# Performance work log

Measured on AMD Instinct MI355X. Metric: run time of the kernel, lower is better.

Reference implementation:

```python
import jax, jax.numpy as jnp
import numpy as np

B, S, J, D = 64, 2048, 25, 3
FEAT_DIM = 128
COMPUTED = 12  # pos(3) + vel(3) + acc(3) + angles(3)
IN_MLP = COMPUTED * J  # 300
HID = FEAT_DIM * 2     # 256
CONN = np.array([(0, 1), (1, 5), (1, 6), (5, 7), (7, 9), (6, 8), (8, 10),
                 (1, 11), (1, 12), (11, 13), (13, 15), (12, 14), (14, 16)], dtype=np.int32)


def setup_inputs() -> dict:
    key = jax.random.key(0)
    ks = jax.random.split(key, 8)
    return {
        "poses": jax.random.normal(ks[0], (B, S, J, D), dtype=jnp.float32),
        "W1": jax.random.normal(ks[1], (IN_MLP, HID), dtype=jnp.float32) * 0.05,
        "b1": jnp.zeros((HID,), jnp.float32),
        "gamma": jnp.ones((HID,), jnp.float32),
        "beta": jnp.zeros((HID,), jnp.float32),
        "running_mean": jnp.zeros((HID,), jnp.float32),
        "running_var": jnp.ones((HID,), jnp.float32),
        "W2": jax.random.normal(ks[2], (HID, FEAT_DIM), dtype=jnp.float32) * 0.05,
        "b2": jnp.zeros((FEAT_DIM,), jnp.float32),
        "joint_weights": jnp.ones((J,), jnp.float32),
    }


def reference(poses, W1, b1, gamma, beta, running_mean, running_var, W2, b2, joint_weights):
    b, s, j, d = poses.shape
    # --- root-centering + max-distance normalization ---
    p = poses - poses[:, :, 0:1, :]
    dist = jnp.linalg.norm(p, axis=-1, keepdims=True)           # [B,S,J,1]
    max_dist = jnp.max(dist, axis=2, keepdims=True)             # [B,S,1,1]
    p = p / (max_dist + 1e-8)
    # --- velocity / acceleration (zero-padded first frames) ---
    zpad = jnp.zeros_like(p[:, :1])
    vel = jnp.concatenate([zpad, p[:, 1:] - p[:, :-1]], axis=1)
    acc = jnp.concatenate([zpad, vel[:, 1:] - vel[:, :-1]], axis=1)
    # --- joint angles: vectorized gather + normalize + acos (replaces B*S*13 python loop) ---
    v1 = p[:, :, CONN[:, 1], :] - p[:, :, CONN[:, 0], :]        # [B,S,13,3]
    vnorm = jnp.maximum(jnp.linalg.norm(v1, axis=-1, keepdims=True), 1e-12)  # F.normalize eps
    ang = jnp.arccos(jnp.clip(v1 / vnorm, -1.0, 1.0))           # [B,S,13,3]
    ang = ang.reshape(b, s, -1)                                 # [B,S,39]
    pad = jnp.zeros((b, s, j * 3 - ang.shape[-1]), ang.dtype)   # pad to J*3=75
    angles = jnp.concatenate([ang, pad], axis=-1).reshape(b, s, j, 3)
    # --- combine, weight, project ---
    feat = jnp.concatenate([p, vel, acc, angles], axis=-1)      # [B,S,J,12]
    feat = feat * joint_weights.reshape(1, 1, j, 1)
    x = feat.reshape(b * s, -1)                                 # [B*S,300]
    x = x @ W1 + b1
    x = gamma * (x - running_mean) / jnp.sqrt(running_var + 1e-5) + beta  # BN eval mode
    x = jax.nn.relu(x)                                          # dropout = identity (eval)
    x = x @ W2 + b2
    return x.reshape(b, s, -1)                                  # [B,S,128]
```

## Files before the change

kernel.cpp:

```cpp
#include <hip/hip_runtime.h>
#include <stdint.h>


#define S_    2048
#define MT_   64
#define TPB   512
#define HID_  256
#define OUT_  128

typedef __attribute__((ext_vector_type(8))) _Float16 half8;
typedef __attribute__((ext_vector_type(4))) float    floatx4;
typedef __attribute__((ext_vector_type(4))) float    f4_t;

#define C0M 0x0ECDB118675110ULL
#define C1M 0x0FDECBA9786540ULL

__device__ __forceinline__ float facos(float x) {
    float ax = fabsf(x);
    float p = fmaf(ax, -0.0187293f, 0.0742610f);
    p = fmaf(ax, p, -0.2121144f);
    p = fmaf(ax, p, 1.5707288f);
    float r = __builtin_amdgcn_sqrtf(1.f - ax) * p;
    return x < 0.f ? 3.14159265358979f - r : r;
}

__global__ void prep_kernel(const float* __restrict__ W1, const float* __restrict__ b1,
                            const float* __restrict__ gamma, const float* __restrict__ beta,
                            const float* __restrict__ rmean, const float* __restrict__ rvar,
                            const float* __restrict__ W2, const float* __restrict__ jw,
                            _Float16* __restrict__ w1p,
                            _Float16* __restrict__ w2p,
                            float* __restrict__ b1p) {
    int bid = blockIdx.x, tid = threadIdx.x;
    if (bid < 352) {
        int k = bid, n = tid;
        float a = gamma[n] * __builtin_amdgcn_rsqf(rvar[n] + 1e-5f);
        float v = 0.f;
        if (k < 288) {
            int d = k / 96, loc = k - d * 96;
            if (loc < 75) {
                int j = loc / 3, c = loc - j * 3;
                const float* Wb = W1 + (j * 12 + c) * HID_ + n;
                float wp = Wb[0], wv = Wb[3 * HID_], wa = Wb[6 * HID_];
                float t = (d == 0) ? (wp + wv + wa) : (d == 1 ? -(wv + 2.f * wa) : wa);
                v = t * a * jw[j];
            }
        } else {
            int q = k - 288;
            if (q < 39) {
                int e = q / 3, aa = q - e * 3;
                v = W1[(e * 12 + 9 + aa) * HID_ + n] * a * jw[e];
            }
        }
        int blk = (k >> 5) * 16 + (n >> 4);
        int off = blk * 512 + (((k >> 3) & 3) * 16 + (n & 15)) * 8 + (k & 7);
        w1p[off] = (_Float16)v;
    } else if (bid < 480) {
        int i2 = (bid - 352) * 256 + tid;
        int k = i2 >> 7, n = i2 & 127;
        int blk = (k >> 5) * 8 + (n >> 4);
        int off = blk * 512 + (((k >> 3) & 3) * 16 + (n & 15)) * 8 + (k & 7);
        w2p[off] = (_Float16)W2[k * OUT_ + n];
    } else {
        int n = tid;
        float a = gamma[n] * __builtin_amdgcn_rsqf(rvar[n] + 1e-5f);
        b1p[n] = fmaf(a, b1[n] - rmean[n], beta[n]);
    }
}

#define L_CCB 0
#define L_AB  11632
#define L_RS  16800
#define L_TOT 33792

__global__ __launch_bounds__(TPB, 8) void pose_mlp(
    const float* __restrict__ poses,
    const _Float16* __restrict__ w1p,
    const _Float16* __restrict__ w2p,
    const float* __restrict__ b1p,
    const float* __restrict__ b2,
    float* __restrict__ out)
{
    __shared__ __align__(16) unsigned char smem[L_TOT];
    const int tid  = threadIdx.x;
    const int lane = tid & 63;
    const int wv   = tid >> 6;
    const int t0   = blockIdx.x * MT_;
    const int s0   = t0 & (S_ - 1);

    _Float16* ccb = (_Float16*)(smem + L_CCB);
    _Float16* ab  = (_Float16*)(smem + L_AB);
    float4*   rs  = (float4*)(smem + L_RS);

    half8 bw[2];
    #pragma unroll
    for (int ni = 0; ni < 2; ni++)
        bw[ni] = *(const half8*)(w1p + (unsigned)(wv * 2 + ni) * 512 + lane * 8);
    float bv[2];
    #pragma unroll
    for (int ni = 0; ni < 2; ni++) bv[ni] = b1p[wv * 32 + ni * 16 + (lane & 15)];
    float c2 = b2[wv * 16 + (lane & 15)];

    if (tid < 96) {
        if (tid < 8)       ccb[66 * 88 + tid] = (_Float16)0.f;
        else if (tid < 32) ab[64 * 40 + (tid - 8)] = (_Float16)0.f;
        else               ab[(tid - 32) * 40 + 39] = (_Float16)0.f;
    }

    #pragma unroll
    for (int r2 = 0; r2 < 2; r2++) {
        int i = r2 * TPB + tid;
        int tt = i >> 4, e = i & 15;
        if (e < 13) {
            const float* P = poses + (size_t)(t0 + tt) * 75;
            int a0 = (int)((C0M >> (4 * e)) & 15) * 3;
            int a1 = (((int)((C1M >> (4 * e)) & 15)) + 1) * 3;
            float vx = P[a1] - P[a0], vy = P[a1+1] - P[a0+1], vz = P[a1+2] - P[a0+2];
            float d  = fmaf(vx, vx, fmaf(vy, vy, vz * vz));
            float inv = __builtin_amdgcn_rcpf(fmaxf(__builtin_amdgcn_sqrtf(d), 1e-12f));
            _Float16* A = ab + tt * 40;
            A[e * 3 + 0] = (_Float16)facos(fminf(fmaxf(vx * inv, -1.f), 1.f));
            A[e * 3 + 1] = (_Float16)facos(fminf(fmaxf(vy * inv, -1.f), 1.f));
            A[e * 3 + 2] = (_Float16)facos(fminf(fmaxf(vz * inv, -1.f), 1.f));
        }
    }

    if (tid < 264) {
        int f = tid >> 2, q = tid & 3;
        int g = t0 + f - 2;
        if (s0 == 0 && f < 2) g = t0;
        const float* P = poses + (size_t)g * 75;
        float r0 = P[0], r1 = P[1], r2 = P[2];
        float m2 = 0.f;
        #pragma unroll
        for (int jj = 0; jj < 7; jj++) {
            int j = q * 7 + jj;
            if (j < 25) {
                float dx = P[j*3]   - r0;
                float dy = P[j*3+1] - r1;
                float dz = P[j*3+2] - r2;
                m2 = fmaxf(m2, fmaf(dx, dx, fmaf(dy, dy, dz * dz)));
            }
        }
        m2 = fmaxf(m2, __shfl_xor(m2, 1));
        m2 = fmaxf(m2, __shfl_xor(m2, 2));
        if (q == 0) {
            float sc = __builtin_amdgcn_rcpf(__builtin_amdgcn_sqrtf(m2) + 1e-8f);
            rs[f] = make_float4(r0, r1, r2, sc);
        }
    }
    __syncthreads();

    #pragma unroll 1
    for (int i = tid; i < 66 * 32; i += TPB) {
        int f = i >> 5, j = i & 31;
        _Float16* C = ccb + f * 88;
        if (j < 25) {
            int g = t0 + f - 2;
            if (s0 == 0 && f < 2) g = t0;
            const float* P = poses + (size_t)g * 75 + j * 3;
            float4 q = rs[f];
            C[j * 3 + 0] = (_Float16)((P[0] - q.x) * q.w);
            C[j * 3 + 1] = (_Float16)((P[1] - q.y) * q.w);
            C[j * 3 + 2] = (_Float16)((P[2] - q.z) * q.w);
        } else {
            int c = 75 + (j - 25) * 2;
            C[c] = (_Float16)0.f;
            if (c + 1 < 88) C[c + 1] = (_Float16)0.f;
        }
    }
    __syncthreads();

    floatx4 acc[4][2];
    #pragma unroll
    for (int mi = 0; mi < 4; mi++)
        #pragma unroll
        for (int ni = 0; ni < 2; ni++)
            acc[mi][ni] = (floatx4){bv[ni], bv[ni], bv[ni], bv[ni]};

    int rowb[4];
    #pragma unroll
    for (int mi = 0; mi < 4; mi++)
        rowb[mi] = (mi * 16 + (lane & 15) + 2) * 88 + (lane >> 4) * 8;

    int koff = 0;
    #pragma unroll 1
    for (int kc = 0; kc < 9; kc++) {
        half8 bn[2];
        #pragma unroll
        for (int ni = 0; ni < 2; ni++)
            bn[ni] = *(const half8*)(w1p + (unsigned)((kc + 1) * 16 + wv * 2 + ni) * 512 + lane * 8);
        half8 af[4];
        #pragma unroll
        for (int mi = 0; mi < 4; mi++)
            af[mi] = *(const half8*)(ccb + rowb[mi] + koff);
        #pragma unroll
        for (int mi = 0; mi < 4; mi++)
            #pragma unroll
            for (int ni = 0; ni < 2; ni++)
                acc[mi][ni] = __builtin_amdgcn_mfma_f32_16x16x32_f16(
                    af[mi], bw[ni], acc[mi][ni], 0, 0, 0);
        bw[0] = bn[0]; bw[1] = bn[1];
        koff += 32; if (kc == 2 || kc == 5) koff -= 184;
    }
    {
        int rowa[4];
        #pragma unroll
        for (int mi = 0; mi < 4; mi++)
            rowa[mi] = (mi * 16 + (lane & 15)) * 40 + (lane >> 4) * 8;
        #pragma unroll
        for (int kc = 9; kc < 11; kc++) {
            half8 bn[2];
            if (kc < 10) {
                #pragma unroll
                for (int ni = 0; ni < 2; ni++)
                    bn[ni] = *(const half8*)(w1p + (unsigned)((kc + 1) * 16 + wv * 2 + ni) * 512 + lane * 8);
            }
            half8 af[4];
            #pragma unroll
            for (int mi = 0; mi < 4; mi++)
                af[mi] = *(const half8*)(ab + rowa[mi] + (kc - 9) * 32);
            #pragma unroll
            for (int mi = 0; mi < 4; mi++)
                #pragma unroll
                for (int ni = 0; ni < 2; ni++)
                    acc[mi][ni] = __builtin_amdgcn_mfma_f32_16x16x32_f16(
                        af[mi], bw[ni], acc[mi][ni], 0, 0, 0);
            if (kc < 10) { bw[0] = bn[0]; bw[1] = bn[1]; }
        }
    }

    half8 bw2 = *(const half8*)(w2p + (unsigned)wv * 512 + lane * 8);

    __syncthreads();

    _Float16* hid = (_Float16*)smem;
    #pragma unroll
    for (int mi = 0; mi < 4; mi++)
        #pragma unroll
        for (int ni = 0; ni < 2; ni++)
            #pragma unroll
            for (int r = 0; r < 4; r++) {
                float v = fmaxf(acc[mi][ni][r], 0.f);
                int m   = mi * 16 + (lane >> 4) * 4 + r;
                int col = wv * 32 + ni * 16 + (lane & 15);
                hid[m * 264 + col] = (_Float16)v;
            }
    __syncthreads();

    floatx4 acc2[4];
    #pragma unroll
    for (int mi = 0; mi < 4; mi++) acc2[mi] = (floatx4){c2, c2, c2, c2};

    #pragma unroll 1
    for (int kc = 0; kc < 8; kc++) {
        half8 bn2;
        if (kc < 7)
            bn2 = *(const half8*)(w2p + (unsigned)((kc + 1) * 8 + wv) * 512 + lane * 8);
        half8 af[4];
        #pragma unroll
        for (int mi = 0; mi < 4; mi++)
            af[mi] = *(const half8*)(hid + (mi * 16 + (lane & 15)) * 264 + kc * 32 + (lane >> 4) * 8);
        #pragma unroll
        for (int mi = 0; mi < 4; mi++)
            acc2[mi] = __builtin_amdgcn_mfma_f32_16x16x32_f16(
                af[mi], bw2, acc2[mi], 0, 0, 0);
        if (kc < 7) bw2 = bn2;
    }
    __syncthreads();

    float* obuf = (float*)smem;
    #pragma unroll
    for (int mi = 0; mi < 4; mi++)
        #pragma unroll
        for (int r = 0; r < 4; r++) {
            int m = mi * 16 + (lane >> 4) * 4 + r;
            obuf[m * 132 + wv * 16 + (lane & 15)] = acc2[mi][r];
        }
    __syncthreads();
    #pragma unroll
    for (int k = 0; k < 4; k++) {
        int idx = k * TPB + tid;
        int row = idx >> 5, c4 = idx & 31;
        f4_t v = *(const f4_t*)(obuf + row * 132 + c4 * 4);
        __builtin_nontemporal_store(v, (f4_t*)out + (size_t)t0 * 32 + idx);
    }
}

extern "C" void kernel_launch(void* const* d_in, const int* in_sizes, int n_in,
                              void* d_out, int out_size, void* d_ws, size_t ws_size,
                              hipStream_t stream) {
    (void)in_sizes; (void)n_in; (void)out_size; (void)ws_size;
    const float* poses = (const float*)d_in[0];
    const float* W1    = (const float*)d_in[1];
    const float* b1    = (const float*)d_in[2];
    const float* gamma = (const float*)d_in[3];
    const float* beta  = (const float*)d_in[4];
    const float* rmean = (const float*)d_in[5];
    const float* rvar  = (const float*)d_in[6];
    const float* W2    = (const float*)d_in[7];
    const float* b2    = (const float*)d_in[8];
    const float* jw    = (const float*)d_in[9];

    _Float16* w1p = (_Float16*)d_ws;
    _Float16* w2p = w1p + 352 * HID_;
    float* b1p = (float*)((char*)d_ws + (352 * HID_ + HID_ * OUT_) * 2);

    prep_kernel<<<481, 256, 0, stream>>>(W1, b1, gamma, beta, rmean, rvar, W2, jw,
                                         w1p, w2p, b1p);
    pose_mlp<<<2048, TPB, 0, stream>>>(poses, w1p, w2p, b1p, b2, (float*)d_out);
}
```

Before: 145.5 us.

## Stage pose tiles in LDS with register prefetch across persistent tile loop

Each block now handles four consecutive 64-row tiles instead of one. Raw pose data for each tile (plus a two-frame halo) is loaded with coalesced float4 reads into a new LDS staging buffer. The next tile's raw data is prefetched into registers while the current tile runs its MFMA work, and is written to LDS at the end of the iteration. The intent is to replace scattered per-element global pose loads with coalesced vector loads and to hide memory latency behind compute. In exchange, LDS use grows by about 20 KB, the occupancy hint drops from 8 to 4 blocks, and the grid shrinks to 512 blocks, which lowers parallelism.

Result: slower. 156.8 us (+7.7%).

```diff
diff --git a/kernel.cpp b/kernel.cpp
--- a/kernel.cpp
+++ b/kernel.cpp
@@ -4,9 +4,11 @@
 
 #define S_    2048
 #define MT_   64
+#define NT_   4
 #define TPB   512
 #define HID_  256
 #define OUT_  128
+#define NF4   1238
 
 typedef __attribute__((ext_vector_type(8))) _Float16 half8;
 typedef __attribute__((ext_vector_type(4))) float    floatx4;
@@ -71,9 +73,10 @@
 #define L_CCB 0
 #define L_AB  11632
 #define L_RS  16800
-#define L_TOT 33792
-
-__global__ __launch_bounds__(TPB, 8) void pose_mlp(
+#define L_RAW 33792
+#define L_TOT (L_RAW + 1240 * 16)
+
+__global__ __launch_bounds__(TPB, 4) void pose_mlp(
     const float* __restrict__ poses,
     const _Float16* __restrict__ w1p,
     const _Float16* __restrict__ w2p,
@@ -85,205 +88,243 @@
     const int tid  = threadIdx.x;
     const int lane = tid & 63;
     const int wv   = tid >> 6;
-    const int t0   = blockIdx.x * MT_;
-    const int s0   = t0 & (S_ - 1);
+    const int tb   = blockIdx.x * (MT_ * NT_);
 
     _Float16* ccb = (_Float16*)(smem + L_CCB);
     _Float16* ab  = (_Float16*)(smem + L_AB);
     float4*   rs  = (float4*)(smem + L_RS);
-
-    half8 bw[2];
-    #pragma unroll
-    for (int ni = 0; ni < 2; ni++)
-        bw[ni] = *(const half8*)(w1p + (unsigned)(wv * 2 + ni) * 512 + lane * 8);
+    float*    raw = (float*)(smem + L_RAW);
+
     float bv[2];
     #pragma unroll
     for (int ni = 0; ni < 2; ni++) bv[ni] = b1p[wv * 32 + ni * 16 + (lane & 15)];
     float c2 = b2[wv * 16 + (lane & 15)];
 
-    if (tid < 96) {
-        if (tid < 8)       ccb[66 * 88 + tid] = (_Float16)0.f;
-        else if (tid < 32) ab[64 * 40 + (tid - 8)] = (_Float16)0.f;
-        else               ab[(tid - 32) * 40 + 39] = (_Float16)0.f;
+    {
+        const long base = (long)tb * 75 - 152;
+        long a0 = base + 4 * (long)tid;
+        if (a0 < 0) a0 = 0;
+        f4_t v0 = *(const f4_t*)(poses + a0);
+        f4_t v1 = *(const f4_t*)(poses + base + 4 * (long)(TPB + tid));
+        f4_t v2 = {};
+        const bool act2 = (2 * TPB + tid) < NF4;
+        if (act2) v2 = *(const f4_t*)(poses + base + 4 * (long)(2 * TPB + tid));
+        *(f4_t*)(raw + 4 * tid) = v0;
+        *(f4_t*)(raw + 4 * (TPB + tid)) = v1;
+        if (act2) *(f4_t*)(raw + 4 * (2 * TPB + tid)) = v2;
     }
 
-    #pragma unroll
-    for (int r2 = 0; r2 < 2; r2++) {
-        int i = r2 * TPB + tid;
-        int tt = i >> 4, e = i & 15;
-        if (e < 13) {
-            const float* P = poses + (size_t)(t0 + tt) * 75;
-            int a0 = (int)((C0M >> (4 * e)) & 15) * 3;
-            int a1 = (((int)((C1M >> (4 * e)) & 15)) + 1) * 3;
-            float vx = P[a1] - P[a0], vy = P[a1+1] - P[a0+1], vz = P[a1+2] - P[a0+2];
-            float d  = fmaf(vx, vx, fmaf(vy, vy, vz * vz));
-            float inv = __builtin_amdgcn_rcpf(fmaxf(__builtin_amdgcn_sqrtf(d), 1e-12f));
-            _Float16* A = ab + tt * 40;
-            A[e * 3 + 0] = (_Float16)facos(fminf(fmaxf(vx * inv, -1.f), 1.f));
-            A[e * 3 + 1] = (_Float16)facos(fminf(fmaxf(vy * inv, -1.f), 1.f));
-            A[e * 3 + 2] = (_Float16)facos(fminf(fmaxf(vz * inv, -1.f), 1.f));
-        }
-    }
-
-    if (tid < 264) {
-        int f = tid >> 2, q = tid & 3;
-        int g = t0 + f - 2;
-        if (s0 == 0 && f < 2) g = t0;
-        const float* P = poses + (size_t)g * 75;
-        float r0 = P[0], r1 = P[1], r2 = P[2];
-        float m2 = 0.f;
-        #pragma unroll
-        for (int jj = 0; jj < 7; jj++) {
-            int j = q * 7 + jj;
+    f4_t sr0, sr1, sr2;
+
+    #pragma unroll 1
+    for (int t = 0; t < NT_; t++) {
+        const int t0 = tb + t * MT_;
+        const int s0 = t0 & (S_ - 1);
+
+        __syncthreads();
+
+        half8 bw[2];
+        #pragma unroll
+        for (int ni = 0; ni < 2; ni++)
+            bw[ni] = *(const half8*)(w1p + (unsigned)(wv * 2 + ni) * 512 + lane * 8);
+
+        if (tid < 96) {
+            if (tid < 8)       ccb[66 * 88 + tid] = (_Float16)0.f;
+            else if (tid < 32) ab[64 * 40 + (tid - 8)] = (_Float16)0.f;
+            else               ab[(tid - 32) * 40 + 39] = (_Float16)0.f;
+        }
+
+        #pragma unroll
+        for (int r2 = 0; r2 < 2; r2++) {
+            int i = r2 * TPB + tid;
+            int tt = i >> 4, e = i & 15;
+            if (e < 13) {
+                const float* R = raw + (tt + 2) * 75 + 2;
+                int a0 = (int)((C0M >> (4 * e)) & 15) * 3;
+                int a1 = (((int)((C1M >> (4 * e)) & 15)) + 1) * 3;
+                float vx = R[a1] - R[a0], vy = R[a1+1] - R[a0+1], vz = R[a1+2] - R[a0+2];
+                float d  = fmaf(vx, vx, fmaf(vy, vy, vz * vz));
+                float inv = __builtin_amdgcn_rcpf(fmaxf(__builtin_amdgcn_sqrtf(d), 1e-12f));
+                _Float16* A = ab + tt * 40;
+                A[e * 3 + 0] = (_Float16)facos(fminf(fmaxf(vx * inv, -1.f), 1.f));
+                A[e * 3 + 1] = (_Float16)facos(fminf(fmaxf(vy * inv, -1.f), 1.f));
+                A[e * 3 + 2] = (_Float16)facos(fminf(fmaxf(vz * inv, -1.f), 1.f));
+            }
+        }
+
+        if (tid < 264) {
+            int f = tid >> 2, q = tid & 3;
+            int fr = (s0 == 0 && f < 2) ? 2 : f;
+            const float* R = raw + fr * 75 + 2;
+            float r0 = R[0], r1 = R[1], r2v = R[2];
+            float m2 = 0.f;
+            #pragma unroll
+            for (int jj = 0; jj < 7; jj++) {
+                int j = q * 7 + jj;
+                if (j < 25) {
+                    float dx = R[j*3]   - r0;
+                    float dy = R[j*3+1] - r1;
+                    float dz = R[j*3+2] - r2v;
+                    m2 = fmaxf(m2, fmaf(dx, dx, fmaf(dy, dy, dz * dz)));
+                }
+            }
+            m2 = fmaxf(m2, __shfl_xor(m2, 1));
+            m2 = fmaxf(m2, __shfl_xor(m2, 2));
+            if (q == 0) {
+                float sc = __builtin_amdgcn_rcpf(__builtin_amdgcn_sqrtf(m2) + 1e-8f);
+                rs[f] = make_float4(r0, r1, r2v, sc);
+            }
+        }
+        __syncthreads();
+
+        #pragma unroll 1
+        for (int i = tid; i < 66 * 32; i += TPB) {
+            int f = i >> 5, j = i & 31;
+            _Float16* C = ccb + f * 88;
             if (j < 25) {
-                float dx = P[j*3]   - r0;
-                float dy = P[j*3+1] - r1;
-                float dz = P[j*3+2] - r2;
-                m2 = fmaxf(m2, fmaf(dx, dx, fmaf(dy, dy, dz * dz)));
-            }
-        }
-        m2 = fmaxf(m2, __shfl_xor(m2, 1));
-        m2 = fmaxf(m2, __shfl_xor(m2, 2));
-        if (q == 0) {
-            float sc = __builtin_amdgcn_rcpf(__builtin_amdgcn_sqrtf(m2) + 1e-8f);
-            rs[f] = make_float4(r0, r1, r2, sc);
-        }
-    }
-    __syncthreads();
-
-    #pragma unroll 1
-    for (int i = tid; i < 66 * 32; i += TPB) {
-        int f = i >> 5, j = i & 31;
-        _Float16* C = ccb + f * 88;
-        if (j < 25) {
-            int g = t0 + f - 2;
-            if (s0 == 0 && f < 2) g = t0;
-            const float* P = poses + (size_t)g * 75 + j * 3;
-            float4 q = rs[f];
-            C[j * 3 + 0] = (_Float16)((P[0] - q.x) * q.w);
-            C[j * 3 + 1] = (_Float16)((P[1] - q.y) * q.w);
-            C[j * 3 + 2] = (_Float16)((P[2] - q.z) * q.w);
-        } else {
-            int c = 75 + (j - 25) * 2;
-            C[c] = (_Float16)0.f;
-            if (c + 1 < 88) C[c + 1] = (_Float16)0.f;
-        }
-    }
-    __syncthreads();
-
-    floatx4 acc[4][2];
-    #pragma unroll
-    for (int mi = 0; mi < 4; mi++)
-        #pragma unroll
-        for (int ni = 0; ni < 2; ni++)
-            acc[mi][ni] = (floatx4){bv[ni], bv[ni], bv[ni], bv[ni]};
-
-    int rowb[4];
-    #pragma unroll
-    for (int mi = 0; mi < 4; mi++)
-        rowb[mi] = (mi * 16 + (lane & 15) + 2) * 88 + (lane >> 4) * 8;
-
-    int koff = 0;
-    #pragma unroll 1
-    for (int kc = 0; kc < 9; kc++) {
-        half8 bn[2];
-        #pragma unroll
-        for (int ni = 0; ni < 2; ni++)
-            bn[ni] = *(const half8*)(w1p + (unsigned)((kc + 1) * 16 + wv * 2 + ni) * 512 + lane * 8);
-        half8 af[4];
+                int fr = (s0 == 0 && f < 2) ? 2 : f;
+                const float* R = raw + fr * 75 + j * 3 + 2;
+                float4 q = rs[f];
+                C[j * 3 + 0] = (_Float16)((R[0] - q.x) * q.w);
+                C[j * 3 + 1] = (_Float16)((R[1] - q.y) * q.w);
+                C[j * 3 + 2] = (_Float16)((R[2] - q.z) * q.w);
+            } else {
+                int c = 75 + (j - 25) * 2;
+                C[c] = (_Float16)0.f;
+                if (c + 1 < 88) C[c + 1] = (_Float16)0.f;
+            }
+        }
+        __syncthreads();
+
+        const bool more = (t < NT_ - 1);
+        if (more) {
+            const long nb = (long)(t0 + MT_) * 75 - 152;
+            sr0 = *(const f4_t*)(poses + nb + 4 * (long)tid);
+            sr1 = *(const f4_t*)(poses + nb + 4 * (long)(TPB + tid));
+            if ((2 * TPB + tid) < NF4)
+                sr2 = *(const f4_t*)(poses + nb + 4 * (long)(2 * TPB + tid));
+        }
+
+        floatx4 acc[4][2];
         #pragma unroll
         for (int mi = 0; mi < 4; mi++)
-            af[mi] = *(const half8*)(ccb + rowb[mi] + koff);
+            #pragma unroll
+            for (int ni = 0; ni < 2; ni++)
+                acc[mi][ni] = (floatx4){bv[ni], bv[ni], bv[ni], bv[ni]};
+
+        int rowb[4];
         #pragma unroll
         for (int mi = 0; mi < 4; mi++)
+            rowb[mi] = (mi * 16 + (lane & 15) + 2) * 88 + (lane >> 4) * 8;
+
+        int koff = 0;
+        #pragma unroll 1
+        for (int kc = 0; kc < 9; kc++) {
+            half8 bn[2];
             #pragma unroll
             for (int ni = 0; ni < 2; ni++)
-                acc[mi][ni] = __builtin_amdgcn_mfma_f32_16x16x32_f16(
-                    af[mi], bw[ni], acc[mi][ni], 0, 0, 0);
-        bw[0] = bn[0]; bw[1] = bn[1];
-        koff += 32; if (kc == 2 || kc == 5) koff -= 184;
-    }
-    {
-        int rowa[4];
-        #pragma unroll
-        for (int mi = 0; mi < 4; mi++)
-            rowa[mi] = (mi * 16 + (lane & 15)) * 40 + (lane >> 4) * 8;
-        #pragma unroll
-        for (int kc = 9; kc < 11; kc++) {
-            half8 bn[2];
-            if (kc < 10) {
-                #pragma unroll
-                for (int ni = 0; ni < 2; ni++)
-                    bn[ni] = *(const half8*)(w1p + (unsigned)((kc + 1) * 16 + wv * 2 + ni) * 512 + lane * 8);
-            }
+                bn[ni] = *(const half8*)(w1p + (unsigned)((kc + 1) * 16 + wv * 2 + ni) * 512 + lane * 8);
             half8 af[4];
             #pragma unroll
             for (int mi = 0; mi < 4; mi++)
-                af[mi] = *(const half8*)(ab + rowa[mi] + (kc - 9) * 32);
+                af[mi] = *(const half8*)(ccb + rowb[mi] + koff);
             #pragma unroll
             for (int mi = 0; mi < 4; mi++)
                 #pragma unroll
                 for (int ni = 0; ni < 2; ni++)
                     acc[mi][ni] = __builtin_amdgcn_mfma_f32_16x16x32_f16(
                         af[mi], bw[ni], acc[mi][ni], 0, 0, 0);
-            if (kc < 10) { bw[0] = bn[0]; bw[1] = bn[1]; }
-        }
-    }
-
-    half8 bw2 = *(const half8*)(w2p + (unsigned)wv * 512 + lane * 8);
-
-    __syncthreads();
-
-    _Float16* hid = (_Float16*)smem;
-    #pragma unroll
-    for (int mi = 0; mi < 4; mi++)
-        #pragma unroll
-        for (int ni = 0; ni < 2; ni++)
+            bw[0] = bn[0]; bw[1] = bn[1];
+            koff += 32; if (kc == 2 || kc == 5) koff -= 184;
+        }
+        {
+            int rowa[4];
+            #pragma unroll
+            for (int mi = 0; mi < 4; mi++)
+                rowa[mi] = (mi * 16 + (lane & 15)) * 40 + (lane >> 4) * 8;
+            #pragma unroll
+            for (int kc = 9; kc < 11; kc++) {
+                half8 bn[2];
+                if (kc < 10) {
+                    #pragma unroll
+                    for (int ni = 0; ni < 2; ni++)
+                        bn[ni] = *(const half8*)(w1p + (unsigned)((kc + 1) * 16 + wv * 2 + ni) * 512 + lane * 8);
+                }
+                half8 af[4];
+                #pragma unroll
+                for (int mi = 0; mi < 4; mi++)
+                    af[mi] = *(const half8*)(ab + rowa[mi] + (kc - 9) * 32);
+                #pragma unroll
+                for (int mi = 0; mi < 4; mi++)
+                    #pragma unroll
+                    for (int ni = 0; ni < 2; ni++)
+                        acc[mi][ni] = __builtin_amdgcn_mfma_f32_16x16x32_f16(
+                            af[mi], bw[ni], acc[mi][ni], 0, 0, 0);
+                if (kc < 10) { bw[0] = bn[0]; bw[1] = bn[1]; }
+            }
+        }
+
+        half8 bw2 = *(const half8*)(w2p + (unsigned)wv * 512 + lane * 8);
+
+        __syncthreads();
+
+        _Float16* hid = (_Float16*)smem;
+        #pragma unroll
+        for (int mi = 0; mi < 4; mi++)
+            #pragma unroll
+            for (int ni = 0; ni < 2; ni++)
+                #pragma unroll
+                for (int r = 0; r < 4; r++) {
+                    float v = fmaxf(acc[mi][ni][r], 0.f);
+                    int m   = mi * 16 + (lane >> 4) * 4 + r;
+                    int col = wv * 32 + ni * 16 + (lane & 15);
+                    hid[m * 264 + col] = (_Float16)v;
+                }
+        __syncthreads();
+
+        floatx4 acc2[4];
+        #pragma unroll
+        for (int mi = 0; mi < 4; mi++) acc2[mi] = (floatx4){c2, c2, c2, c2};
+
+        #pragma unroll 1
+        for (int kc = 0; kc < 8; kc++) {
+            half8 bn2;
+            if (kc < 7)
+                bn2 = *(const half8*)(w2p + (unsigned)((kc + 1) * 8 + wv) * 512 + lane * 8);
+            half8 af[4];
+            #pragma unroll
+            for (int mi = 0; mi < 4; mi++)
+                af[mi] = *(const half8*)(hid + (mi * 16 + (lane & 15)) * 264 + kc * 32 + (lane >> 4) * 8);
+            #pragma unroll
+            for (int mi = 0; mi < 4; mi++)
+                acc2[mi] = __builtin_amdgcn_mfma_f32_16x16x32_f16(
+                    af[mi], bw2, acc2[mi], 0, 0, 0);
+            if (kc < 7) bw2 = bn2;
+        }
+        __syncthreads();
+
+        float* obuf = (float*)smem;
+        #pragma unroll
+        for (int mi = 0; mi < 4; mi++)
             #pragma unroll
             for (int r = 0; r < 4; r++) {
-                float v = fmaxf(acc[mi][ni][r], 0.f);
-                int m   = mi * 16 + (lane >> 4) * 4 + r;
-                int col = wv * 32 + ni * 16 + (lane & 15);
-                hid[m * 264 + col] = (_Float16)v;
-            }
-    __syncthreads();
-
-    floatx4 acc2[4];
-    #pragma unroll
-    for (int mi = 0; mi < 4; mi++) acc2[mi] = (floatx4){c2, c2, c2, c2};
-
-    #pragma unroll 1
-    for (int kc = 0; kc < 8; kc++) {
-        half8 bn2;
-        if (kc < 7)
-            bn2 = *(const half8*)(w2p + (unsigned)((kc + 1) * 8 + wv) * 512 + lane * 8);
-        half8 af[4];
-        #pragma unroll
-        for (int mi = 0; mi < 4; mi++)
-            af[mi] = *(const half8*)(hid + (mi * 16 + (lane & 15)) * 264 + kc * 32 + (lane >> 4) * 8);
-        #pragma unroll
-        for (int mi = 0; mi < 4; mi++)
-            acc2[mi] = __builtin_amdgcn_mfma_f32_16x16x32_f16(
-                af[mi], bw2, acc2[mi], 0, 0, 0);
-        if (kc < 7) bw2 = bn2;
-    }
-    __syncthreads();
-
-    float* obuf = (float*)smem;
-    #pragma unroll
-    for (int mi = 0; mi < 4; mi++)
-        #pragma unroll
-        for (int r = 0; r < 4; r++) {
-            int m = mi * 16 + (lane >> 4) * 4 + r;
-            obuf[m * 132 + wv * 16 + (lane & 15)] = acc2[mi][r];
-        }
-    __syncthreads();
-    #pragma unroll
-    for (int k = 0; k < 4; k++) {
-        int idx = k * TPB + tid;
-        int row = idx >> 5, c4 = idx & 31;
-        f4_t v = *(const f4_t*)(obuf + row * 132 + c4 * 4);
-        __builtin_nontemporal_store(v, (f4_t*)out + (size_t)t0 * 32 + idx);
+                int m = mi * 16 + (lane >> 4) * 4 + r;
+                obuf[m * 132 + wv * 16 + (lane & 15)] = acc2[mi][r];
+            }
+        __syncthreads();
+        #pragma unroll
+        for (int k = 0; k < 4; k++) {
+            int idx = k * TPB + tid;
+            int row = idx >> 5, c4 = idx & 31;
+            f4_t v = *(const f4_t*)(obuf + row * 132 + c4 * 4);
+            __builtin_nontemporal_store(v, (f4_t*)out + (size_t)t0 * 32 + idx);
+        }
+
+        if (more) {
+            *(f4_t*)(raw + 4 * tid) = sr0;
+            *(f4_t*)(raw + 4 * (TPB + tid)) = sr1;
+            if ((2 * TPB + tid) < NF4) *(f4_t*)(raw + 4 * (2 * TPB + tid)) = sr2;
+        }
     }
 }
 
@@ -308,5 +349,5 @@
 
     prep_kernel<<<481, 256, 0, stream>>>(W1, b1, gamma, beta, rmean, rvar, W2, jw,
                                          w1p, w2p, b1p);
-    pose_mlp<<<2048, TPB, 0, stream>>>(poses, w1p, w2p, b1p, b2, (float*)d_out);
+    pose_mlp<<<512, TPB, 0, stream>>>(poses, w1p, w2p, b1p, b2, (float*)d_out);
 }
```
